# Optimization experiments

Hardware: AMD Instinct MI355X
Metric: run time of the kernel (lower is better)

The kernel has to match this reference:

```python
import jax, jax.numpy as jnp
import numpy as np

# ---- model constants (match init_kwargs) ----
N_USERS = 100_000
N_ITEMS = 50_000
N_ENTITIES = 200_000          # items are entities [0, N_ITEMS)
N_REL = 20                    # relations after the +1 shift; rel_weight has N_REL-1 rows
EMB = 64
HOPS = 2
MARGIN_CCL = 0.8
NUM_NEG = 64
ANGLE_W = 0.1
ANGLE_DROP = 0.5              # eval-mode Dropout(ones)*rate == constant rate scaling
N_EDGES = 1_000_000
NNZ = 1_000_000
N_TRIPLETS = 200_000
BATCH = 4096
EPS = 1e-6


def _l2norm(x):
    # torch F.normalize(dim=-1, eps=1e-12)
    return x / jnp.maximum(jnp.linalg.norm(x, axis=-1, keepdims=True), 1e-12)


def setup_inputs() -> dict:
    key = jax.random.key(0)
    ks = jax.random.split(key, 13)
    # xavier_uniform bounds: sqrt(6/(fan_in+fan_out))
    b_all = float(np.sqrt(6.0 / (N_USERS + N_ENTITIES + EMB)))
    b_cf = float(np.sqrt(6.0 / (N_ITEMS + EMB)))
    b_rel = float(np.sqrt(6.0 / (N_REL - 1 + EMB)))
    all_embed = jax.random.uniform(ks[0], (N_USERS + N_ENTITIES, EMB), jnp.float32, -b_all, b_all)
    item_emb_cf = jax.random.uniform(ks[1], (N_ITEMS, EMB), jnp.float32, -b_cf, b_cf)
    rel_weight = jax.random.uniform(ks[2], (N_REL - 1, EMB), jnp.float32, -b_rel, b_rel)
    # D^{-1/2} A row-normalized positive values
    interact_vals = jax.random.uniform(ks[3], (NNZ,), jnp.float32, 0.01, 0.3)
    user = jax.random.randint(ks[4], (BATCH,), 0, N_USERS)
    pos_item = jax.random.randint(ks[5], (BATCH,), 0, N_ITEMS)
    neg_item = jax.random.randint(ks[6], (BATCH, NUM_NEG), 0, N_ITEMS)
    edge_index = jax.random.randint(ks[7], (2, N_EDGES), 0, N_ENTITIES)
    edge_type = jax.random.randint(ks[8], (N_EDGES,), 1, N_REL)  # relations already +1 shifted
    interact_rows = jax.random.randint(ks[9], (NNZ,), 0, N_USERS)
    interact_cols = jax.random.randint(ks[10], (NNZ,), 0, N_ITEMS)  # URM cols live in item range
    triplet_h = jax.random.randint(ks[11], (N_TRIPLETS,), 0, N_ENTITIES)
    triplet_t = jax.random.randint(ks[12], (N_TRIPLETS,), 0, N_ITEMS)
    return dict(all_embed=all_embed, item_emb_cf=item_emb_cf, rel_weight=rel_weight,
                interact_vals=interact_vals, user=user, pos_item=pos_item, neg_item=neg_item,
                edge_index=edge_index, edge_type=edge_type, interact_rows=interact_rows,
                interact_cols=interact_cols, triplet_h=triplet_h, triplet_t=triplet_t)


def _gcn(user_emb, entity_emb, item_cf, rel_weight, edge_index, edge_type, rows, cols, vals):
    """Multi-hop HAKG GraphConv: relation-gated KG scatter-mean + sparse user/CF aggregation."""
    head, tail = edge_index[0], edge_index[1]
    ent_res, usr_res, cf_res = entity_emb, user_emb, item_cf
    cnt = jax.ops.segment_sum(jnp.ones(head.shape, entity_emb.dtype), head, N_ENTITIES)
    denom = jnp.maximum(cnt, 1.0)[:, None]            # scatter_mean denominator
    rel_e = rel_weight[edge_type - 1]                 # [E, D]
    for _ in range(HOPS):
        # KG aggregate: entity_agg[h] = mean_{(h,r,t)} entity[t] * rel[r]
        neigh = entity_emb[tail] * rel_e              # [E, D]
        entity_agg = jax.ops.segment_sum(neigh, head, N_ENTITIES) / denom
        # user aggregate: sparse interact_mat @ entity_emb
        user_agg = jax.ops.segment_sum(vals[:, None] * entity_emb[cols], rows, N_USERS)
        # CF branch (LightGCN-style): R @ item_cf then R^T @ (...)
        u_cf = jax.ops.segment_sum(vals[:, None] * item_cf[cols], rows, N_USERS)
        item_agg_cf = jax.ops.segment_sum(vals[:, None] * u_cf[rows], cols, N_ITEMS)
        entity_emb = _l2norm(entity_agg)
        user_emb = _l2norm(user_agg)
        item_cf = _l2norm(item_agg_cf)
        ent_res = ent_res + entity_emb
        usr_res = usr_res + user_emb
        cf_res = cf_res + item_cf
    return ent_res, usr_res, cf_res


def _half_aperture(u):
    K = 0.1
    sqnu = jnp.clip(jnp.sum(u * u, -1), 0.0, 1.0 - EPS)
    return jnp.arcsin(jnp.clip(K * (1.0 - sqnu) / jnp.sqrt(sqnu), -1.0 + EPS, 1.0 - EPS))


def _angle_at_u(u, v):
    nu = jnp.linalg.norm(u, axis=-1)
    nv = jnp.linalg.norm(v, axis=-1)
    dp = jnp.sum(u * v, -1)
    ed = jnp.linalg.norm(u - v, axis=-1)
    num = dp * (1.0 + nu ** 2) - nu ** 2 * (1.0 + nv ** 2)
    den = nu * ed * jnp.sqrt(jnp.clip(1.0 + nv ** 2 * nu ** 2 - 2.0 * dp, EPS, None)) + EPS
    return jnp.arccos(jnp.clip(num / den, -1.0 + EPS, 1.0 - EPS))


def _contrastive_loss(u_e, pos_e, neg_e, pos_cf, neg_cf):
    B = u_e.shape[0]
    u, p, n = _l2norm(u_e), _l2norm(pos_e), _l2norm(neg_e)
    pcf, ncf = _l2norm(pos_cf), _l2norm(neg_cf)
    ui_pos = jax.nn.relu(2.0 - (jnp.sum(u * p, -1) + jnp.sum(u * pcf, -1)))
    ub = jnp.repeat(u, NUM_NEG, axis=0)               # [B*K, D]
    def neg_loss(nn_):
        s = jax.nn.relu(jnp.sum(ub * nn_, -1) - MARGIN_CCL).reshape(B, NUM_NEG)
        return jnp.sum(s, -1) / (jnp.sum(s > 0, -1).astype(s.dtype) + 1e-5)
    return jnp.mean(ui_pos + neg_loss(n) + neg_loss(ncf))


def reference(all_embed, item_emb_cf, rel_weight, interact_vals, user, pos_item, neg_item,
              edge_index, edge_type, interact_rows, interact_cols, triplet_h, triplet_t):
    user_emb = all_embed[:N_USERS]
    entity_emb = all_embed[N_USERS:]
    ent_g, usr_g, cf_g = _gcn(user_emb, entity_emb, item_emb_cf, rel_weight,
                              edge_index, edge_type, interact_rows, interact_cols, interact_vals)
    flat_neg = neg_item.reshape(-1)
    u_e = usr_g[user]
    loss1 = _contrastive_loss(u_e, ent_g[pos_item], ent_g[flat_neg], cf_g[pos_item], cf_g[flat_neg])
    # angle (hierarchy) loss, vectorized over all cross-type triplets
    hs = entity_emb[triplet_h] * ANGLE_DROP
    ts = entity_emb[triplet_t] * ANGLE_DROP
    angle_half = jax.nn.relu(_angle_at_u(hs, ts) - _half_aperture(hs))
    loss2 = ANGLE_W * jnp.sum(angle_half) / N_TRIPLETS
    return loss1 + loss2
```

## Files before the change

kernel.cpp:

```cpp
#include <hip/hip_runtime.h>
#include <math.h>

#define N_USERS    100000
#define N_ITEMS    50000
#define N_ENTITIES 200000
#define N_REL      20
#define EMB        64
#define HOPS       2
#define MARGIN_CCL 0.8f
#define NUM_NEG    64
#define ANGLE_W    0.1f
#define ANGLE_DROP 0.5f
#define N_EDGES    1000000
#define NNZ        1000000
#define N_TRIPLETS 200000
#define BATCH      4096
#define EPSF       1e-6f

#define TILE1 4096
#define NBUCK 196
#define BCAP  9216
#define ACAP  8192
#define HBLK  ((N_EDGES + TILE1 - 1) / TILE1)
#define P1B   (3 * HBLK)
#define KGB   (N_ENTITIES / 32)
#define USERB (N_USERS / 16)
#define ITEMB ((N_ITEMS + 31) / 32)
#define ANGB  (N_TRIPLETS / 32)
#define LOSSB (BATCH / 4)
#define CONVE (N_ENTITIES * 16 / 256)
#define CONVI (N_ITEMS * 16 / 256)

typedef _Float16 half4_t __attribute__((ext_vector_type(4)));
typedef _Float16 half8_t __attribute__((ext_vector_type(8)));
typedef float float8_t __attribute__((ext_vector_type(8)));

__device__ inline float4 h2f(half4_t h) {
    return make_float4((float)h.x, (float)h.y, (float)h.z, (float)h.w);
}
__device__ inline half4_t f2h(float4 f) {
    half4_t h; h.x = (_Float16)f.x; h.y = (_Float16)f.y;
    h.z = (_Float16)f.z; h.w = (_Float16)f.w; return h;
}
__device__ inline float8_t h8_to_f8(half8_t h) { return __builtin_convertvector(h, float8_t); }
__device__ inline half8_t f8_to_h8(float8_t f) { return __builtin_convertvector(f, half8_t); }
__device__ inline half8_t h8_zero() {
    half8_t z;
    #pragma unroll
    for (int i = 0; i < 8; ++i) z[i] = (_Float16)0.0f;
    return z;
}
__device__ inline float sum_sq8(float8_t f) {
    float s = 0.f;
    #pragma unroll
    for (int i = 0; i < 8; ++i) s += f[i] * f[i];
    return s;
}
__device__ inline float dot8(float8_t a, float8_t b) {
    float s = 0.f;
    #pragma unroll
    for (int i = 0; i < 8; ++i) s += a[i] * b[i];
    return s;
}
__device__ inline float8_t f8_from2(float4 lo, float4 hi) {
    float8_t f;
    f[0] = lo.x; f[1] = lo.y; f[2] = lo.z; f[3] = lo.w;
    f[4] = hi.x; f[5] = hi.y; f[6] = hi.z; f[7] = hi.w;
    return f;
}
__device__ inline float grp_red8(float v) {
    v += __shfl_xor(v, 1, 64); v += __shfl_xor(v, 2, 64); v += __shfl_xor(v, 4, 64);
    return v;
}
__device__ inline float dot4(float4 a, float4 b) {
    return a.x * b.x + a.y * b.y + a.z * b.z + a.w * b.w;
}
__device__ inline float grp_red16(float v) {
    v += __shfl_xor(v, 1, 64); v += __shfl_xor(v, 2, 64);
    v += __shfl_xor(v, 4, 64); v += __shfl_xor(v, 8, 64);
    return v;
}
__device__ inline float cross_grp_scalar(float v) {
    v += __shfl_xor(v, 16, 64); v += __shfl_xor(v, 32, 64);
    return v;
}

__global__ void __launch_bounds__(256) prep_kernel(
        const float4* __restrict__ ent0, const float4* __restrict__ cf0,
        half4_t* __restrict__ ent_a, half4_t* __restrict__ comb_a,
        int* __restrict__ bcur_e, int* __restrict__ bcur_u, int* __restrict__ bcur_i) {
    int bx = blockIdx.x, t = threadIdx.x;
    if (bx < CONVE) { int i = bx * 256 + t; ent_a[i] = f2h(ent0[i]); return; }
    bx -= CONVE;
    if (bx < CONVI) {
        int i = bx * 256 + t;
        int row = i >> 4, o4 = i & 15;
        comb_a[row * 32 + o4] = f2h(ent0[i]);
        return;
    }
    bx -= CONVI;
    if (bx < CONVI) {
        int i = bx * 256 + t;
        int row = i >> 4, o4 = i & 15;
        comb_a[row * 32 + 16 + o4] = f2h(cf0[i]);
        return;
    }
    if (t < NBUCK) {
        bcur_e[t] = t * ACAP;
        bcur_u[t] = t * ACAP;
        bcur_i[t] = t * ACAP;
    }
}

__device__ inline void angle_body(int ablk, int t, const half8_t* __restrict__ ent_h,
                                  const int* __restrict__ th, const int* __restrict__ tt,
                                  float* sb, float* __restrict__ l2blk) {
    int o = t & 7;
    int grp = t >> 3;
    int trip = ablk * 32 + grp;
    int h = th[trip], t2 = tt[trip];
    float8_t hv = h8_to_f8(ent_h[h * 8 + o]);
    float8_t tv = h8_to_f8(ent_h[t2 * 8 + o]);
    hv *= ANGLE_DROP;
    tv *= ANGLE_DROP;
    float8_t dv = hv - tv;
    float s_hh = grp_red8(sum_sq8(hv));
    float s_tt = grp_red8(sum_sq8(tv));
    float s_ht = grp_red8(dot8(hv, tv));
    float s_dd = grp_red8(sum_sq8(dv));
    if (o == 0) {
        float nu = sqrtf(s_hh);
        float ed = sqrtf(s_dd);
        float sqnu = fminf(fmaxf(s_hh, 0.0f), 1.0f - EPSF);
        float ha_arg = fminf(fmaxf(0.1f * (1.0f - sqnu) / sqrtf(sqnu), -1.0f + EPSF), 1.0f - EPSF);
        float half_ap = asinf(ha_arg);
        float num = s_ht * (1.0f + s_hh) - s_hh * (1.0f + s_tt);
        float den = nu * ed * sqrtf(fmaxf(1.0f + s_tt * s_hh - 2.0f * s_ht, EPSF)) + EPSF;
        float ang = acosf(fminf(fmaxf(num / den, -1.0f + EPSF), 1.0f - EPSF));
        sb[grp] = fmaxf(ang - half_ap, 0.0f);
    }
    __syncthreads();
    if (t == 0) {
        float tot = 0.f;
        #pragma unroll
        for (int i = 0; i < 32; ++i) tot += sb[i];
        l2blk[ablk] = tot;
    }
}

__global__ void __launch_bounds__(256) phase1_angle(
        const int* __restrict__ head, const int* __restrict__ tail,
        const int* __restrict__ etype, const int* __restrict__ rows,
        const int* __restrict__ cols, const float* __restrict__ vals,
        int* __restrict__ bcur_e, int* __restrict__ bcur_u, int* __restrict__ bcur_i,
        int* __restrict__ keys_e, int* __restrict__ kg_pay,
        int2* __restrict__ u_pay, int2* __restrict__ i_pay,
        const half8_t* __restrict__ ent_a, const int* __restrict__ th,
        const int* __restrict__ tt, float* __restrict__ l2blk) {
    __shared__ int2 pay_st[TILE1];
    __shared__ int lhist[256], lstart[256], lcur[256], gbase[256];
    __shared__ float sb[32];
    int bx = blockIdx.x, t = threadIdx.x;
    if (bx >= P1B) {
        angle_body(bx - P1B, t, ent_a, th, tt, sb, l2blk);
        return;
    }
    int seg = bx / HBLK;
    int tb  = bx % HBLK;
    int tstart = tb * TILE1;
    int valid = min(TILE1, N_EDGES - tstart);
    const int* karr = (seg == 0) ? head : (seg == 1) ? rows : cols;
    int shift = (seg == 0) ? 10 : (seg == 1) ? 9 : 8;
    int* bcur = (seg == 0) ? bcur_e : (seg == 1) ? bcur_u : bcur_i;
    lhist[t] = 0;
    __syncthreads();
    for (int i = t; i < valid; i += 256) atomicAdd(&lhist[karr[tstart + i] >> shift], 1);
    __syncthreads();
    int v = lhist[t];
    lstart[t] = v;
    __syncthreads();
    for (int d = 1; d < 256; d <<= 1) {
        int x = (t >= d) ? lstart[t - d] : 0;
        __syncthreads();
        lstart[t] += x;
        __syncthreads();
    }
    int excl = lstart[t] - v;
    lstart[t] = excl;
    lcur[t] = excl;
    gbase[t] = atomicAdd(&bcur[t], v);
    __syncthreads();
    if (seg == 0) {
        int* key_st = (int*)pay_st;
        int* ps = key_st + TILE1;
        for (int i = t; i < valid; i += 256) {
            int h = head[tstart + i];
            int p = tail[tstart + i] | ((etype[tstart + i] - 1) << 18);
            int sp = atomicAdd(&lcur[h >> 10], 1);
            key_st[sp] = h;
            ps[sp] = p;
        }
        __syncthreads();
        for (int j = t; j < valid; j += 256) {
            int k = key_st[j];
            int b = k >> 10;
            int pos = gbase[b] + (j - lstart[b]);
            keys_e[pos] = k;
            kg_pay[pos] = ps[j];
        }
    } else {
        int2* pay = (seg == 1) ? u_pay : i_pay;
        for (int i = t; i < valid; i += 256) {
            int k = karr[tstart + i];
            int px;
            if (seg == 1) px = cols[tstart + i] | ((k & 511) << 16);
            else          px = rows[tstart + i] | ((k & 255) << 17);
            int2 p = make_int2(px, __float_as_int(vals[tstart + i]));
            int sp = atomicAdd(&lcur[k >> shift], 1);
            pay_st[sp] = p;
        }
        __syncthreads();
        for (int j = t; j < valid; j += 256) {
            int2 p = pay_st[j];
            int key = (seg == 1) ? ((p.x >> 16) & 511) : ((p.x >> 17) & 255);
            int b = (gbase[0], 0);
            (void)b;
            int lo = 0, hi = 255;
            while (lo < hi) {
                int mid = (lo + hi + 1) >> 1;
                if (lstart[mid] <= j) lo = mid; else hi = mid - 1;
            }
            int bb = lo;
            int pos = gbase[bb] + (j - lstart[bb]);
            pay[pos] = p;
        }
    }
}

__global__ void __launch_bounds__(256) phase2_all(
        const int* __restrict__ bcur_e, const int* __restrict__ keys_e,
        int* __restrict__ kg_pay, int* __restrict__ off_e,
        const int* __restrict__ bcur_u, int2* __restrict__ u_pay, int* __restrict__ off_u,
        const int* __restrict__ bcur_i, int2* __restrict__ i_pay, int* __restrict__ off_i) {
    __shared__ int hist[1024];
    __shared__ int s[256];
    __shared__ int2 lout2[BCAP];
    int seg = blockIdx.x / NBUCK;
    int b   = blockIdx.x % NBUCK;
    int t = threadIdx.x;
    int bins  = (seg == 0) ? 1024 : (seg == 1) ? 512 : 256;
    int shift = (seg == 0) ? 10 : (seg == 1) ? 9 : 8;
    int n_rows = (seg == 0) ? N_ENTITIES : (seg == 1) ? N_USERS : N_ITEMS;
    const int* bcur = (seg == 0) ? bcur_e : (seg == 1) ? bcur_u : bcur_i;
    int* off = (seg == 0) ? off_e : (seg == 1) ? off_u : off_i;
    int rs = b << shift;
    int re = min(rs + bins, n_rows);
    int nr = re - rs;
    int base = b * ACAP;
    int len = bcur[b] - base;
    for (int r = t; r < bins; r += 256) hist[r] = 0;
    __syncthreads();
    if (seg == 0) {
        for (int j = t; j < len; j += 256) atomicAdd(&hist[keys_e[base + j] - rs], 1);
    } else if (seg == 1) {
        for (int j = t; j < len; j += 256) atomicAdd(&hist[(u_pay[base + j].x >> 16) & 511], 1);
    } else {
        for (int j = t; j < len; j += 256) atomicAdd(&hist[(i_pay[base + j].x >> 17) & 255], 1);
    }
    __syncthreads();
    int own = bins >> 8;
    int c[4]; int tot = 0;
    #pragma unroll 4
    for (int i = 0; i < own; ++i) { c[i] = hist[t * own + i]; tot += c[i]; }
    s[t] = tot;
    __syncthreads();
    for (int d = 1; d < 256; d <<= 1) {
        int x = (t >= d) ? s[t - d] : 0;
        __syncthreads();
        s[t] += x;
        __syncthreads();
    }
    int run = s[t] - tot;
    #pragma unroll 4
    for (int i = 0; i < own; ++i) { hist[t * own + i] = run; run += c[i]; }
    __syncthreads();
    for (int r = t; r < nr; r += 256) off[rs + b + r] = base + hist[r];
    if (t == 0) off[rs + b + nr] = base + len;
    __syncthreads();
    if (seg == 0) {
        int* lo = (int*)lout2;
        for (int j = t; j < len; j += 256) {
            int k = keys_e[base + j];
            int slot = atomicAdd(&hist[k - rs], 1);
            lo[slot] = kg_pay[base + j];
        }
        __syncthreads();
        for (int j = t; j < len; j += 256) kg_pay[base + j] = lo[j];
    } else {
        int2* pay = (seg == 1) ? u_pay : i_pay;
        int sh = (seg == 1) ? 16 : 17;
        int msk = (seg == 1) ? 511 : 255;
        for (int j = t; j < len; j += 256) {
            int2 p = pay[base + j];
            int slot = atomicAdd(&hist[(p.x >> sh) & msk], 1);
            lout2[slot] = p;
        }
        __syncthreads();
        for (int j = t; j < len; j += 256) pay[base + j] = lout2[j];
    }
}

__device__ inline void kg_body(int bid, int t, const int* __restrict__ off,
                               const int* __restrict__ pack, half8_t* srel,
                               const float* __restrict__ relw,
                               const half8_t* __restrict__ src, half8_t* __restrict__ dst,
                               half8_t* __restrict__ comb_nxt, half8_t* __restrict__ res,
                               const float4* __restrict__ res_init, int first, int last) {
    if (t < (N_REL - 1) * 8) {
        int rel = t >> 3, o = t & 7;
        const float4* r4 = (const float4*)relw;
        srel[rel * 9 + o] = f8_to_h8(f8_from2(r4[rel * 16 + o * 2], r4[rel * 16 + o * 2 + 1]));
    }
    __syncthreads();
    int row = bid * 32 + (t >> 3);
    int o = t & 7;
    int idx = row + (row >> 10);
    int s = off[idx], e = off[idx + 1];
    half8_t acc = h8_zero();
    int k = s;
    for (; k + 2 <= e; k += 2) {
        int p0 = pack[k], p1 = pack[k + 1];
        half8_t a0 = src[(p0 & 0x3FFFF) * 8 + o];
        half8_t b0 = srel[(p0 >> 18) * 9 + o];
        half8_t a1 = src[(p1 & 0x3FFFF) * 8 + o];
        half8_t b1 = srel[(p1 >> 18) * 9 + o];
        acc += a0 * b0;
        acc += a1 * b1;
    }
    if (k < e) {
        int p0 = pack[k];
        acc += src[(p0 & 0x3FFFF) * 8 + o] * srel[(p0 >> 18) * 9 + o];
    }
    float8_t f = h8_to_f8(acc);
    f *= 1.0f / fmaxf((float)(e - s), 1.0f);
    float ss = grp_red8(sum_sq8(f));
    f *= 1.0f / fmaxf(sqrtf(ss), 1e-12f);
    half8_t oh = f8_to_h8(f);
    dst[row * 8 + o] = oh;
    if (row < N_ITEMS) {
        if (!last) comb_nxt[row * 16 + o] = oh;
        float8_t rr;
        if (first) rr = f8_from2(res_init[row * 16 + o * 2], res_init[row * 16 + o * 2 + 1]);
        else       rr = h8_to_f8(res[row * 8 + o]);
        rr += f;
        if (last) {
            float s2 = grp_red8(sum_sq8(rr));
            rr *= 1.0f / fmaxf(sqrtf(s2), 1e-12f);
        }
        res[row * 8 + o] = f8_to_h8(rr);
    }
}

__device__ inline void user_body(int bid, int t, const int* __restrict__ off,
                                 const int2* __restrict__ u_pack,
                                 const half8_t* __restrict__ comb,
                                 half8_t* __restrict__ usr_res,
                                 const float4* __restrict__ res_init,
                                 half8_t* __restrict__ ucf, int first, int last) {
    int row = bid * 16 + (t >> 4);
    int o = t & 15;
    int idx = row + (row >> 9);
    int s = off[idx], e = off[idx + 1];
    half8_t acc = h8_zero();
    int k = s;
    for (; k + 2 <= e; k += 2) {
        int2 p0 = u_pack[k], p1 = u_pack[k + 1];
        _Float16 v0 = (_Float16)__int_as_float(p0.y);
        _Float16 v1 = (_Float16)__int_as_float(p1.y);
        acc += comb[(p0.x & 0xFFFF) * 16 + o] * v0;
        acc += comb[(p1.x & 0xFFFF) * 16 + o] * v1;
    }
    if (k < e) {
        int2 p0 = u_pack[k];
        acc += comb[(p0.x & 0xFFFF) * 16 + o] * (_Float16)__int_as_float(p0.y);
    }
    float8_t f = h8_to_f8(acc);
    float ss = grp_red8(sum_sq8(f));
    if (o < 8) {
        float rn = 1.0f / fmaxf(sqrtf(ss), 1e-12f);
        float8_t rr;
        if (first) rr = f8_from2(res_init[row * 16 + o * 2], res_init[row * 16 + o * 2 + 1]);
        else       rr = h8_to_f8(usr_res[row * 8 + o]);
        rr += f * rn;
        if (last) {
            float s2 = grp_red8(sum_sq8(rr));
            rr *= 1.0f / fmaxf(sqrtf(s2), 1e-12f);
        }
        usr_res[row * 8 + o] = f8_to_h8(rr);
    } else {
        ucf[row * 8 + (o - 8)] = acc;
    }
}

__device__ inline void item_body(int bid, int t, const int* __restrict__ off,
                                 const int2* __restrict__ i_pack,
                                 const half8_t* __restrict__ ucf,
                                 half8_t* __restrict__ comb_nxt, half8_t* __restrict__ res,
                                 const float4* __restrict__ res_init, int first, int last) {
    int row = bid * 32 + (t >> 3);
    int o = t & 7;
    if (row >= N_ITEMS) return;
    int idx = row + (row >> 8);
    int s = off[idx], e = off[idx + 1];
    half8_t acc = h8_zero();
    int k = s;
    for (; k + 2 <= e; k += 2) {
        int2 p0 = i_pack[k], p1 = i_pack[k + 1];
        _Float16 v0 = (_Float16)__int_as_float(p0.y);
        _Float16 v1 = (_Float16)__int_as_float(p1.y);
        acc += ucf[(p0.x & 0x1FFFF) * 8 + o] * v0;
        acc += ucf[(p1.x & 0x1FFFF) * 8 + o] * v1;
    }
    if (k < e) {
        int2 p0 = i_pack[k];
        acc += ucf[(p0.x & 0x1FFFF) * 8 + o] * (_Float16)__int_as_float(p0.y);
    }
    float8_t f = h8_to_f8(acc);
    float ss = grp_red8(sum_sq8(f));
    f *= 1.0f / fmaxf(sqrtf(ss), 1e-12f);
    if (!last) comb_nxt[row * 16 + 8 + o] = f8_to_h8(f);
    float8_t rr;
    if (first) rr = f8_from2(res_init[row * 16 + o * 2], res_init[row * 16 + o * 2 + 1]);
    else       rr = h8_to_f8(res[row * 8 + o]);
    rr += f;
    if (last) {
        float s2 = grp_red8(sum_sq8(rr));
        rr *= 1.0f / fmaxf(sqrtf(s2), 1e-12f);
    }
    res[row * 8 + o] = f8_to_h8(rr);
}

__device__ inline void loss_ent_body(int b, int t, const int* __restrict__ user,
                                     const int* __restrict__ pos, const int* __restrict__ neg,
                                     const half4_t* __restrict__ usr4,
                                     const half4_t* __restrict__ ent4,
                                     float* __restrict__ dpe, float* __restrict__ l1pe) {
    int lane = t & 63;
    int g = lane >> 4, q = lane & 15;
    int uid = user[b], pid = pos[b];
    float4 u = h2f(usr4[uid * 16 + q]);
    float4 p = h2f(ent4[pid * 16 + q]);
    float dpe_v = grp_red16(dot4(u, p));
    float sum_n = 0.f, cnt_n = 0.f;
    const int* nb = neg + b * NUM_NEG;
    for (int j = 0; j < NUM_NEG; j += 8) {
        int n0 = nb[j + g], n1 = nb[j + 4 + g];
        float dn0 = grp_red16(dot4(u, h2f(ent4[n0 * 16 + q])));
        float dn1 = grp_red16(dot4(u, h2f(ent4[n1 * 16 + q])));
        float s0 = fmaxf(dn0 - MARGIN_CCL, 0.f); sum_n += s0; if (s0 > 0.f) cnt_n += 1.f;
        float s1 = fmaxf(dn1 - MARGIN_CCL, 0.f); sum_n += s1; if (s1 > 0.f) cnt_n += 1.f;
    }
    sum_n = cross_grp_scalar(sum_n); cnt_n = cross_grp_scalar(cnt_n);
    if (lane == 0) {
        dpe[b] = dpe_v;
        l1pe[b] = sum_n / (cnt_n + 1e-5f);
    }
}

__global__ void __launch_bounds__(256) loss_cf_kernel(
        const int* __restrict__ user, const int* __restrict__ pos,
        const int* __restrict__ neg, const half4_t* __restrict__ usr4,
        const half4_t* __restrict__ cf4, const float* __restrict__ dpe,
        const float* __restrict__ l1pe, float* __restrict__ l1p) {
    int b = blockIdx.x * 4 + (threadIdx.x >> 6);
    int lane = threadIdx.x & 63;
    int g = lane >> 4, q = lane & 15;
    int uid = user[b], pid = pos[b];
    float4 u = h2f(usr4[uid * 16 + q]);
    float4 pc = h2f(cf4[pid * 16 + q]);
    float dpc = grp_red16(dot4(u, pc));
    float sum_c = 0.f, cnt_c = 0.f;
    const int* nb = neg + b * NUM_NEG;
    for (int j = 0; j < NUM_NEG; j += 8) {
        int n0 = nb[j + g], n1 = nb[j + 4 + g];
        float dc0 = grp_red16(dot4(u, h2f(cf4[n0 * 16 + q])));
        float dc1 = grp_red16(dot4(u, h2f(cf4[n1 * 16 + q])));
        float t0 = fmaxf(dc0 - MARGIN_CCL, 0.f); sum_c += t0; if (t0 > 0.f) cnt_c += 1.f;
        float t1 = fmaxf(dc1 - MARGIN_CCL, 0.f); sum_c += t1; if (t1 > 0.f) cnt_c += 1.f;
    }
    sum_c = cross_grp_scalar(sum_c); cnt_c = cross_grp_scalar(cnt_c);
    if (lane == 0) {
        float ui_pos = fmaxf(2.0f - dpe[b] - dpc, 0.0f);
        l1p[b] = ui_pos + l1pe[b] + sum_c / (cnt_c + 1e-5f);
    }
}

__global__ void __launch_bounds__(256) fused_h0(
        const int* __restrict__ off_e, const int* __restrict__ kg_pack,
        const float* __restrict__ relw, const half8_t* __restrict__ ent_a,
        half8_t* __restrict__ ent_b, half8_t* __restrict__ comb_b,
        half8_t* __restrict__ ent_res, const float4* __restrict__ ent0f,
        const int* __restrict__ off_u, const int2* __restrict__ u_pack,
        const half8_t* __restrict__ comb_a, half8_t* __restrict__ usr_res,
        const float4* __restrict__ usr0f, half8_t* __restrict__ ucf) {
    __shared__ half8_t srel[(N_REL - 1) * 9];
    int bx = blockIdx.x, t = threadIdx.x;
    if (bx < KGB) {
        kg_body(bx, t, off_e, kg_pack, srel, relw, ent_a, ent_b, comb_b, ent_res, ent0f, 1, 0);
    } else {
        user_body(bx - KGB, t, off_u, u_pack, comb_a, usr_res, usr0f, ucf, 1, 0);
    }
}

__global__ void __launch_bounds__(256) fused_ik(
        const int* __restrict__ off_e, const int* __restrict__ kg_pack,
        const float* __restrict__ relw, const half8_t* __restrict__ ent_b,
        half8_t* __restrict__ ent_a, half8_t* __restrict__ ent_res,
        const float4* __restrict__ ent0f,
        const int* __restrict__ off_i, const int2* __restrict__ i_pack,
        const half8_t* __restrict__ ucf, half8_t* __restrict__ comb_b,
        half8_t* __restrict__ cf_res, const float4* __restrict__ cf0f) {
    __shared__ half8_t srel[(N_REL - 1) * 9];
    int bx = blockIdx.x, t = threadIdx.x;
    if (bx < KGB) {
        kg_body(bx, t, off_e, kg_pack, srel, relw, ent_b, ent_a, comb_b, ent_res, ent0f, 0, 1);
    } else {
        item_body(bx - KGB, t, off_i, i_pack, ucf, comb_b, cf_res, cf0f, 1, 0);
    }
}

__global__ void __launch_bounds__(256) user_h1(
        const int* __restrict__ off_u, const int2* __restrict__ u_pack,
        const half8_t* __restrict__ comb_b, half8_t* __restrict__ usr_res,
        const float4* __restrict__ usr0f, half8_t* __restrict__ ucf) {
    user_body(blockIdx.x, threadIdx.x, off_u, u_pack, comb_b, usr_res, usr0f, ucf, 0, 1);
}

__global__ void __launch_bounds__(256) fused_item_loss(
        const int* __restrict__ off_i, const int2* __restrict__ i_pack,
        const half8_t* __restrict__ ucf, half8_t* __restrict__ comb_unused,
        half8_t* __restrict__ cf_res, const float4* __restrict__ cf0f,
        const int* __restrict__ user, const int* __restrict__ pos,
        const int* __restrict__ neg, const half4_t* __restrict__ usr4,
        const half4_t* __restrict__ ent4, float* __restrict__ dpe,
        float* __restrict__ l1pe) {
    int bx = blockIdx.x, t = threadIdx.x;
    if (bx < ITEMB) {
        item_body(bx, t, off_i, i_pack, ucf, comb_unused, cf_res, cf0f, 0, 1);
    } else {
        int b = (bx - ITEMB) * 4 + (t >> 6);
        loss_ent_body(b, t, user, pos, neg, usr4, ent4, dpe, l1pe);
    }
}

__global__ void finalize_kernel(const float* __restrict__ l1p, const float* __restrict__ l2b,
                                float* __restrict__ out) {
    __shared__ float sb[1024];
    float a1 = 0.f;
    for (int i = threadIdx.x; i < BATCH; i += 1024) a1 += l1p[i];
    float a2 = 0.f;
    for (int i = threadIdx.x; i < ANGB; i += 1024) a2 += l2b[i];
    sb[threadIdx.x] = a1 / (float)BATCH + ANGLE_W * a2 / (float)N_TRIPLETS;
    __syncthreads();
    for (int s = 512; s > 0; s >>= 1) {
        if (threadIdx.x < s) sb[threadIdx.x] += sb[threadIdx.x + s];
        __syncthreads();
    }
    if (threadIdx.x == 0) out[0] = sb[0];
}

extern "C" void kernel_launch(void* const* d_in, const int* in_sizes, int n_in,
                              void* d_out, int out_size, void* d_ws, size_t ws_size,
                              hipStream_t stream) {
    const float* all_embed = (const float*)d_in[0];
    const float* item_cf0  = (const float*)d_in[1];
    const float* relw      = (const float*)d_in[2];
    const float* vals      = (const float*)d_in[3];
    const int* user        = (const int*)d_in[4];
    const int* pos_item    = (const int*)d_in[5];
    const int* neg_item    = (const int*)d_in[6];
    const int* edge_head   = (const int*)d_in[7];
    const int* edge_tail   = edge_head + N_EDGES;
    const int* etype       = (const int*)d_in[8];
    const int* irows       = (const int*)d_in[9];
    const int* icols       = (const int*)d_in[10];
    const int* th          = (const int*)d_in[11];
    const int* tt          = (const int*)d_in[12];
    float* out             = (float*)d_out;

    char* base = (char*)d_ws;
    size_t woff = 0;
    auto alloc = [&](size_t bytes) -> void* {
        void* p = base + woff;
        woff = (woff + bytes + 255) & ~(size_t)255;
        return p;
    };
    half8_t* ent_a   = (half8_t*)alloc((size_t)N_ENTITIES * EMB * 2);
    half8_t* ent_b   = (half8_t*)alloc((size_t)N_ENTITIES * EMB * 2);
    half8_t* comb_a  = (half8_t*)alloc((size_t)N_ITEMS * EMB * 4);
    half8_t* comb_b  = (half8_t*)alloc((size_t)N_ITEMS * EMB * 4);
    half8_t* ucf     = (half8_t*)alloc((size_t)N_USERS * EMB * 2);
    half8_t* ent_res = (half8_t*)alloc((size_t)N_ITEMS * EMB * 2);
    half8_t* usr_res = (half8_t*)alloc((size_t)N_USERS * EMB * 2);
    half8_t* cf_res  = (half8_t*)alloc((size_t)N_ITEMS * EMB * 2);
    int2* u_pack     = (int2*)alloc((size_t)NBUCK * ACAP * 8);
    int2* i_pack     = (int2*)alloc((size_t)NBUCK * ACAP * 8);
    int* kg_pack     = (int*)alloc((size_t)NBUCK * ACAP * 4);
    int* keys_e      = (int*)alloc((size_t)NBUCK * ACAP * 4);
    float* l1p       = (float*)alloc((size_t)BATCH * 4);
    float* dpe       = (float*)alloc((size_t)BATCH * 4);
    float* l1pe      = (float*)alloc((size_t)BATCH * 4);
    float* l2blk     = (float*)alloc((size_t)ANGB * 4);
    int* off_e       = (int*)alloc((size_t)(N_ENTITIES + NBUCK + 1) * 4);
    int* off_u       = (int*)alloc((size_t)(N_USERS + NBUCK + 1) * 4);
    int* off_i       = (int*)alloc((size_t)(N_ITEMS + NBUCK + 1) * 4);
    int* bcur_e      = (int*)alloc(256 * 4);
    int* bcur_u      = (int*)alloc(256 * 4);
    int* bcur_i      = (int*)alloc(256 * 4);

    const float* ent0 = all_embed + (size_t)N_USERS * EMB;

    prep_kernel<<<CONVE + 2 * CONVI + 1, 256, 0, stream>>>(
        (const float4*)ent0, (const float4*)item_cf0, (half4_t*)ent_a, (half4_t*)comb_a,
        bcur_e, bcur_u, bcur_i);
    phase1_angle<<<P1B + ANGB, 256, 0, stream>>>(
        edge_head, edge_tail, etype, irows, icols, vals,
        bcur_e, bcur_u, bcur_i, keys_e, kg_pack, u_pack, i_pack,
        ent_a, th, tt, l2blk);
    phase2_all<<<3 * NBUCK, 256, 0, stream>>>(bcur_e, keys_e, kg_pack, off_e,
                                              bcur_u, u_pack, off_u,
                                              bcur_i, i_pack, off_i);
    fused_h0<<<KGB + USERB, 256, 0, stream>>>(
        off_e, kg_pack, relw, ent_a, ent_b, comb_b, ent_res, (const float4*)ent0,
        off_u, u_pack, comb_a, usr_res, (const float4*)all_embed, ucf);
    fused_ik<<<KGB + ITEMB, 256, 0, stream>>>(
        off_e, kg_pack, relw, ent_b, ent_a, ent_res, (const float4*)ent0,
        off_i, i_pack, ucf, comb_b, cf_res, (const float4*)item_cf0);
    user_h1<<<USERB, 256, 0, stream>>>(off_u, u_pack, comb_b, usr_res,
                                       (const float4*)all_embed, ucf);
    fused_item_loss<<<ITEMB + LOSSB, 256, 0, stream>>>(
        off_i, i_pack, ucf, comb_a, cf_res, (const float4*)item_cf0,
        user, pos_item, neg_item, (const half4_t*)usr_res, (const half4_t*)ent_res,
        dpe, l1pe);
    loss_cf_kernel<<<LOSSB, 256, 0, stream>>>(user, pos_item, neg_item,
                                              (const half4_t*)usr_res, (const half4_t*)cf_res,
                                              dpe, l1pe, l1p);
    finalize_kernel<<<1, 1024, 0, stream>>>(l1p, l2blk, out);
}
```

Measured before the change: 415.5 us.

## Compute final-hop user embeddings only for batch users and restrict hop-2 KG to items

The final-hop KG aggregation now runs only over item rows, since only items are consumed downstream. The user aggregation over entity embeddings is computed just for the 4096 batch users, both hops at once, instead of for all 100k users. The combined entity/CF buffer is split into separate CF half buffers, and the user-CF and item-CF passes are regrouped into different fused kernels. This cuts gather traffic and block count substantially, but it changes the fp16 rounding order of the user residual and recomputes work for users that appear more than once in the batch.

```diff
diff --git a/kernel.cpp b/kernel.cpp
--- a/kernel.cpp
+++ b/kernel.cpp
@@ -24,8 +24,9 @@
 #define HBLK  ((N_EDGES + TILE1 - 1) / TILE1)
 #define P1B   (3 * HBLK)
 #define KGB   (N_ENTITIES / 32)
-#define USERB (N_USERS / 16)
+#define UCFB  (N_USERS / 32)
 #define ITEMB ((N_ITEMS + 31) / 32)
+#define UBB   (BATCH / 32)
 #define ANGB  (N_TRIPLETS / 32)
 #define LOSSB (BATCH / 4)
 #define CONVE (N_ENTITIES * 16 / 256)
@@ -87,24 +88,12 @@
 
 __global__ void __launch_bounds__(256) prep_kernel(
         const float4* __restrict__ ent0, const float4* __restrict__ cf0,
-        half4_t* __restrict__ ent_a, half4_t* __restrict__ comb_a,
+        half4_t* __restrict__ ent_a, half4_t* __restrict__ cf16_a,
         int* __restrict__ bcur_e, int* __restrict__ bcur_u, int* __restrict__ bcur_i) {
     int bx = blockIdx.x, t = threadIdx.x;
     if (bx < CONVE) { int i = bx * 256 + t; ent_a[i] = f2h(ent0[i]); return; }
     bx -= CONVE;
-    if (bx < CONVI) {
-        int i = bx * 256 + t;
-        int row = i >> 4, o4 = i & 15;
-        comb_a[row * 32 + o4] = f2h(ent0[i]);
-        return;
-    }
-    bx -= CONVI;
-    if (bx < CONVI) {
-        int i = bx * 256 + t;
-        int row = i >> 4, o4 = i & 15;
-        comb_a[row * 32 + 16 + o4] = f2h(cf0[i]);
-        return;
-    }
+    if (bx < CONVI) { int i = bx * 256 + t; cf16_a[i] = f2h(cf0[i]); return; }
     if (t < NBUCK) {
         bcur_e[t] = t * ACAP;
         bcur_u[t] = t * ACAP;
@@ -222,9 +211,6 @@
         __syncthreads();
         for (int j = t; j < valid; j += 256) {
             int2 p = pay_st[j];
-            int key = (seg == 1) ? ((p.x >> 16) & 511) : ((p.x >> 17) & 255);
-            int b = (gbase[0], 0);
-            (void)b;
             int lo = 0, hi = 255;
             while (lo < hi) {
                 int mid = (lo + hi + 1) >> 1;
@@ -310,12 +296,11 @@
     }
 }
 
-__device__ inline void kg_body(int bid, int t, const int* __restrict__ off,
-                               const int* __restrict__ pack, half8_t* srel,
-                               const float* __restrict__ relw,
-                               const half8_t* __restrict__ src, half8_t* __restrict__ dst,
-                               half8_t* __restrict__ comb_nxt, half8_t* __restrict__ res,
-                               const float4* __restrict__ res_init, int first, int last) {
+__device__ inline void kg0_body(int bid, int t, const int* __restrict__ off,
+                                const int* __restrict__ pack, half8_t* srel,
+                                const float* __restrict__ relw,
+                                const half8_t* __restrict__ src, half8_t* __restrict__ dst,
+                                half8_t* __restrict__ res, const float4* __restrict__ res_init) {
     if (t < (N_REL - 1) * 8) {
         int rel = t >> 3, o = t & 7;
         const float4* r4 = (const float4*)relw;
@@ -345,30 +330,61 @@
     f *= 1.0f / fmaxf((float)(e - s), 1.0f);
     float ss = grp_red8(sum_sq8(f));
     f *= 1.0f / fmaxf(sqrtf(ss), 1e-12f);
-    half8_t oh = f8_to_h8(f);
-    dst[row * 8 + o] = oh;
+    dst[row * 8 + o] = f8_to_h8(f);
     if (row < N_ITEMS) {
-        if (!last) comb_nxt[row * 16 + o] = oh;
-        float8_t rr;
-        if (first) rr = f8_from2(res_init[row * 16 + o * 2], res_init[row * 16 + o * 2 + 1]);
-        else       rr = h8_to_f8(res[row * 8 + o]);
+        float8_t rr = f8_from2(res_init[row * 16 + o * 2], res_init[row * 16 + o * 2 + 1]);
         rr += f;
-        if (last) {
-            float s2 = grp_red8(sum_sq8(rr));
-            rr *= 1.0f / fmaxf(sqrtf(s2), 1e-12f);
-        }
         res[row * 8 + o] = f8_to_h8(rr);
     }
 }
 
-__device__ inline void user_body(int bid, int t, const int* __restrict__ off,
-                                 const int2* __restrict__ u_pack,
-                                 const half8_t* __restrict__ comb,
-                                 half8_t* __restrict__ usr_res,
-                                 const float4* __restrict__ res_init,
-                                 half8_t* __restrict__ ucf, int first, int last) {
-    int row = bid * 16 + (t >> 4);
-    int o = t & 15;
+__device__ inline void kg2_body(int bid, int t, const int* __restrict__ off,
+                                const int* __restrict__ pack, half8_t* srel,
+                                const float* __restrict__ relw,
+                                const half8_t* __restrict__ src, half8_t* __restrict__ res) {
+    if (t < (N_REL - 1) * 8) {
+        int rel = t >> 3, o = t & 7;
+        const float4* r4 = (const float4*)relw;
+        srel[rel * 9 + o] = f8_to_h8(f8_from2(r4[rel * 16 + o * 2], r4[rel * 16 + o * 2 + 1]));
+    }
+    __syncthreads();
+    int row = bid * 32 + (t >> 3);
+    if (row >= N_ITEMS) return;
+    int o = t & 7;
+    int idx = row + (row >> 10);
+    int s = off[idx], e = off[idx + 1];
+    half8_t acc = h8_zero();
+    int k = s;
+    for (; k + 2 <= e; k += 2) {
+        int p0 = pack[k], p1 = pack[k + 1];
+        half8_t a0 = src[(p0 & 0x3FFFF) * 8 + o];
+        half8_t b0 = srel[(p0 >> 18) * 9 + o];
+        half8_t a1 = src[(p1 & 0x3FFFF) * 8 + o];
+        half8_t b1 = srel[(p1 >> 18) * 9 + o];
+        acc += a0 * b0;
+        acc += a1 * b1;
+    }
+    if (k < e) {
+        int p0 = pack[k];
+        acc += src[(p0 & 0x3FFFF) * 8 + o] * srel[(p0 >> 18) * 9 + o];
+    }
+    float8_t f = h8_to_f8(acc);
+    f *= 1.0f / fmaxf((float)(e - s), 1.0f);
+    float ss = grp_red8(sum_sq8(f));
+    f *= 1.0f / fmaxf(sqrtf(ss), 1e-12f);
+    float8_t rr = h8_to_f8(res[row * 8 + o]);
+    rr += f;
+    float s2 = grp_red8(sum_sq8(rr));
+    rr *= 1.0f / fmaxf(sqrtf(s2), 1e-12f);
+    res[row * 8 + o] = f8_to_h8(rr);
+}
+
+__device__ inline void ucf_body(int bid, int t, const int* __restrict__ off,
+                                const int2* __restrict__ u_pack,
+                                const half8_t* __restrict__ cf16,
+                                half8_t* __restrict__ ucf) {
+    int row = bid * 32 + (t >> 3);
+    int o = t & 7;
     int idx = row + (row >> 9);
     int s = off[idx], e = off[idx + 1];
     half8_t acc = h8_zero();
@@ -377,35 +393,66 @@
         int2 p0 = u_pack[k], p1 = u_pack[k + 1];
         _Float16 v0 = (_Float16)__int_as_float(p0.y);
         _Float16 v1 = (_Float16)__int_as_float(p1.y);
-        acc += comb[(p0.x & 0xFFFF) * 16 + o] * v0;
-        acc += comb[(p1.x & 0xFFFF) * 16 + o] * v1;
+        acc += cf16[(p0.x & 0xFFFF) * 8 + o] * v0;
+        acc += cf16[(p1.x & 0xFFFF) * 8 + o] * v1;
     }
     if (k < e) {
         int2 p0 = u_pack[k];
-        acc += comb[(p0.x & 0xFFFF) * 16 + o] * (_Float16)__int_as_float(p0.y);
-    }
-    float8_t f = h8_to_f8(acc);
-    float ss = grp_red8(sum_sq8(f));
-    if (o < 8) {
-        float rn = 1.0f / fmaxf(sqrtf(ss), 1e-12f);
-        float8_t rr;
-        if (first) rr = f8_from2(res_init[row * 16 + o * 2], res_init[row * 16 + o * 2 + 1]);
-        else       rr = h8_to_f8(usr_res[row * 8 + o]);
-        rr += f * rn;
-        if (last) {
-            float s2 = grp_red8(sum_sq8(rr));
-            rr *= 1.0f / fmaxf(sqrtf(s2), 1e-12f);
-        }
-        usr_res[row * 8 + o] = f8_to_h8(rr);
-    } else {
-        ucf[row * 8 + (o - 8)] = acc;
-    }
+        acc += cf16[(p0.x & 0xFFFF) * 8 + o] * (_Float16)__int_as_float(p0.y);
+    }
+    ucf[row * 8 + o] = acc;
+}
+
+__device__ inline void ubatch_body(int bid, int t, const int* __restrict__ user,
+                                   const int* __restrict__ off,
+                                   const int2* __restrict__ u_pack,
+                                   const half8_t* __restrict__ ent_a,
+                                   const half8_t* __restrict__ ent_b,
+                                   const float4* __restrict__ usr0f,
+                                   half8_t* __restrict__ usr_b) {
+    int g = t >> 3, o = t & 7;
+    int b = bid * 32 + g;
+    int uid = user[b];
+    int idx = uid + (uid >> 9);
+    int s = off[idx], e = off[idx + 1];
+    half8_t acc1 = h8_zero(), acc2 = h8_zero();
+    int k = s;
+    for (; k + 2 <= e; k += 2) {
+        int2 p0 = u_pack[k], p1 = u_pack[k + 1];
+        int c0 = (p0.x & 0xFFFF) * 8 + o;
+        int c1 = (p1.x & 0xFFFF) * 8 + o;
+        _Float16 v0 = (_Float16)__int_as_float(p0.y);
+        _Float16 v1 = (_Float16)__int_as_float(p1.y);
+        acc1 += ent_a[c0] * v0;
+        acc2 += ent_b[c0] * v0;
+        acc1 += ent_a[c1] * v1;
+        acc2 += ent_b[c1] * v1;
+    }
+    if (k < e) {
+        int2 p0 = u_pack[k];
+        int c0 = (p0.x & 0xFFFF) * 8 + o;
+        _Float16 v0 = (_Float16)__int_as_float(p0.y);
+        acc1 += ent_a[c0] * v0;
+        acc2 += ent_b[c0] * v0;
+    }
+    float8_t f1 = h8_to_f8(acc1);
+    float ss1 = grp_red8(sum_sq8(f1));
+    f1 *= 1.0f / fmaxf(sqrtf(ss1), 1e-12f);
+    float8_t u0 = f8_from2(usr0f[uid * 16 + o * 2], usr0f[uid * 16 + o * 2 + 1]);
+    float8_t r1 = h8_to_f8(f8_to_h8(u0 + f1));
+    float8_t f2 = h8_to_f8(acc2);
+    float ss2 = grp_red8(sum_sq8(f2));
+    f2 *= 1.0f / fmaxf(sqrtf(ss2), 1e-12f);
+    float8_t r = r1 + f2;
+    float s3 = grp_red8(sum_sq8(r));
+    r *= 1.0f / fmaxf(sqrtf(s3), 1e-12f);
+    usr_b[b * 8 + o] = f8_to_h8(r);
 }
 
 __device__ inline void item_body(int bid, int t, const int* __restrict__ off,
                                  const int2* __restrict__ i_pack,
                                  const half8_t* __restrict__ ucf,
-                                 half8_t* __restrict__ comb_nxt, half8_t* __restrict__ res,
+                                 half8_t* __restrict__ cf_nxt, half8_t* __restrict__ res,
                                  const float4* __restrict__ res_init, int first, int last) {
     int row = bid * 32 + (t >> 3);
     int o = t & 7;
@@ -428,7 +475,7 @@
     float8_t f = h8_to_f8(acc);
     float ss = grp_red8(sum_sq8(f));
     f *= 1.0f / fmaxf(sqrtf(ss), 1e-12f);
-    if (!last) comb_nxt[row * 16 + 8 + o] = f8_to_h8(f);
+    if (!last) cf_nxt[row * 8 + o] = f8_to_h8(f);
     float8_t rr;
     if (first) rr = f8_from2(res_init[row * 16 + o * 2], res_init[row * 16 + o * 2 + 1]);
     else       rr = h8_to_f8(res[row * 8 + o]);
@@ -440,15 +487,15 @@
     res[row * 8 + o] = f8_to_h8(rr);
 }
 
-__device__ inline void loss_ent_body(int b, int t, const int* __restrict__ user,
+__device__ inline void loss_ent_body(int b, int t,
                                      const int* __restrict__ pos, const int* __restrict__ neg,
-                                     const half4_t* __restrict__ usr4,
+                                     const half4_t* __restrict__ usrb4,
                                      const half4_t* __restrict__ ent4,
                                      float* __restrict__ dpe, float* __restrict__ l1pe) {
     int lane = t & 63;
     int g = lane >> 4, q = lane & 15;
-    int uid = user[b], pid = pos[b];
-    float4 u = h2f(usr4[uid * 16 + q]);
+    int pid = pos[b];
+    float4 u = h2f(usrb4[b * 16 + q]);
     float4 p = h2f(ent4[pid * 16 + q]);
     float dpe_v = grp_red16(dot4(u, p));
     float sum_n = 0.f, cnt_n = 0.f;
@@ -468,15 +515,15 @@
 }
 
 __global__ void __launch_bounds__(256) loss_cf_kernel(
-        const int* __restrict__ user, const int* __restrict__ pos,
-        const int* __restrict__ neg, const half4_t* __restrict__ usr4,
-        const half4_t* __restrict__ cf4, const float* __restrict__ dpe,
-        const float* __restrict__ l1pe, float* __restrict__ l1p) {
+        const int* __restrict__ pos, const int* __restrict__ neg,
+        const half4_t* __restrict__ usrb4, const half4_t* __restrict__ cf4,
+        const float* __restrict__ dpe, const float* __restrict__ l1pe,
+        float* __restrict__ l1p) {
     int b = blockIdx.x * 4 + (threadIdx.x >> 6);
     int lane = threadIdx.x & 63;
     int g = lane >> 4, q = lane & 15;
-    int uid = user[b], pid = pos[b];
-    float4 u = h2f(usr4[uid * 16 + q]);
+    int pid = pos[b];
+    float4 u = h2f(usrb4[b * 16 + q]);
     float4 pc = h2f(cf4[pid * 16 + q]);
     float dpc = grp_red16(dot4(u, pc));
     float sum_c = 0.f, cnt_c = 0.f;
@@ -498,59 +545,60 @@
 __global__ void __launch_bounds__(256) fused_h0(
         const int* __restrict__ off_e, const int* __restrict__ kg_pack,
         const float* __restrict__ relw, const half8_t* __restrict__ ent_a,
-        half8_t* __restrict__ ent_b, half8_t* __restrict__ comb_b,
-        half8_t* __restrict__ ent_res, const float4* __restrict__ ent0f,
+        half8_t* __restrict__ ent_b, half8_t* __restrict__ ent_res,
+        const float4* __restrict__ ent0f,
         const int* __restrict__ off_u, const int2* __restrict__ u_pack,
-        const half8_t* __restrict__ comb_a, half8_t* __restrict__ usr_res,
-        const float4* __restrict__ usr0f, half8_t* __restrict__ ucf) {
+        const half8_t* __restrict__ cf16_a, half8_t* __restrict__ ucf) {
     __shared__ half8_t srel[(N_REL - 1) * 9];
     int bx = blockIdx.x, t = threadIdx.x;
     if (bx < KGB) {
-        kg_body(bx, t, off_e, kg_pack, srel, relw, ent_a, ent_b, comb_b, ent_res, ent0f, 1, 0);
+        kg0_body(bx, t, off_e, kg_pack, srel, relw, ent_a, ent_b, ent_res, ent0f);
     } else {
-        user_body(bx - KGB, t, off_u, u_pack, comb_a, usr_res, usr0f, ucf, 1, 0);
+        ucf_body(bx - KGB, t, off_u, u_pack, cf16_a, ucf);
     }
 }
 
 __global__ void __launch_bounds__(256) fused_ik(
         const int* __restrict__ off_e, const int* __restrict__ kg_pack,
         const float* __restrict__ relw, const half8_t* __restrict__ ent_b,
-        half8_t* __restrict__ ent_a, half8_t* __restrict__ ent_res,
-        const float4* __restrict__ ent0f,
+        half8_t* __restrict__ ent_res,
         const int* __restrict__ off_i, const int2* __restrict__ i_pack,
-        const half8_t* __restrict__ ucf, half8_t* __restrict__ comb_b,
-        half8_t* __restrict__ cf_res, const float4* __restrict__ cf0f) {
+        const half8_t* __restrict__ ucf, half8_t* __restrict__ cf16_b,
+        half8_t* __restrict__ cf_res, const float4* __restrict__ cf0f,
+        const int* __restrict__ user, const int* __restrict__ off_u,
+        const int2* __restrict__ u_pack, const half8_t* __restrict__ ent_a,
+        const float4* __restrict__ usr0f, half8_t* __restrict__ usr_b) {
     __shared__ half8_t srel[(N_REL - 1) * 9];
     int bx = blockIdx.x, t = threadIdx.x;
-    if (bx < KGB) {
-        kg_body(bx, t, off_e, kg_pack, srel, relw, ent_b, ent_a, comb_b, ent_res, ent0f, 0, 1);
+    if (bx < ITEMB) {
+        kg2_body(bx, t, off_e, kg_pack, srel, relw, ent_b, ent_res);
+    } else if (bx < 2 * ITEMB) {
+        item_body(bx - ITEMB, t, off_i, i_pack, ucf, cf16_b, cf_res, cf0f, 1, 0);
     } else {
-        item_body(bx - KGB, t, off_i, i_pack, ucf, comb_b, cf_res, cf0f, 1, 0);
-    }
-}
-
-__global__ void __launch_bounds__(256) user_h1(
+        ubatch_body(bx - 2 * ITEMB, t, user, off_u, u_pack, ent_a, ent_b, usr0f, usr_b);
+    }
+}
+
+__global__ void __launch_bounds__(256) fused_u1_loss(
         const int* __restrict__ off_u, const int2* __restrict__ u_pack,
-        const half8_t* __restrict__ comb_b, half8_t* __restrict__ usr_res,
-        const float4* __restrict__ usr0f, half8_t* __restrict__ ucf) {
-    user_body(blockIdx.x, threadIdx.x, off_u, u_pack, comb_b, usr_res, usr0f, ucf, 0, 1);
-}
-
-__global__ void __launch_bounds__(256) fused_item_loss(
+        const half8_t* __restrict__ cf16_b, half8_t* __restrict__ ucf,
+        const int* __restrict__ pos, const int* __restrict__ neg,
+        const half4_t* __restrict__ usrb4, const half4_t* __restrict__ ent4,
+        float* __restrict__ dpe, float* __restrict__ l1pe) {
+    int bx = blockIdx.x, t = threadIdx.x;
+    if (bx < UCFB) {
+        ucf_body(bx, t, off_u, u_pack, cf16_b, ucf);
+    } else {
+        int b = (bx - UCFB) * 4 + (t >> 6);
+        loss_ent_body(b, t, pos, neg, usrb4, ent4, dpe, l1pe);
+    }
+}
+
+__global__ void __launch_bounds__(256) item_h1(
         const int* __restrict__ off_i, const int2* __restrict__ i_pack,
-        const half8_t* __restrict__ ucf, half8_t* __restrict__ comb_unused,
-        half8_t* __restrict__ cf_res, const float4* __restrict__ cf0f,
-        const int* __restrict__ user, const int* __restrict__ pos,
-        const int* __restrict__ neg, const half4_t* __restrict__ usr4,
-        const half4_t* __restrict__ ent4, float* __restrict__ dpe,
-        float* __restrict__ l1pe) {
-    int bx = blockIdx.x, t = threadIdx.x;
-    if (bx < ITEMB) {
-        item_body(bx, t, off_i, i_pack, ucf, comb_unused, cf_res, cf0f, 0, 1);
-    } else {
-        int b = (bx - ITEMB) * 4 + (t >> 6);
-        loss_ent_body(b, t, user, pos, neg, usr4, ent4, dpe, l1pe);
-    }
+        const half8_t* __restrict__ ucf, half8_t* __restrict__ cf_res,
+        const float4* __restrict__ cf0f) {
+    item_body(blockIdx.x, threadIdx.x, off_i, i_pack, ucf, (half8_t*)0, cf_res, cf0f, 0, 1);
 }
 
 __global__ void finalize_kernel(const float* __restrict__ l1p, const float* __restrict__ l2b,
@@ -597,12 +645,12 @@
     };
     half8_t* ent_a   = (half8_t*)alloc((size_t)N_ENTITIES * EMB * 2);
     half8_t* ent_b   = (half8_t*)alloc((size_t)N_ENTITIES * EMB * 2);
-    half8_t* comb_a  = (half8_t*)alloc((size_t)N_ITEMS * EMB * 4);
-    half8_t* comb_b  = (half8_t*)alloc((size_t)N_ITEMS * EMB * 4);
+    half8_t* cf16_a  = (half8_t*)alloc((size_t)N_ITEMS * EMB * 2);
+    half8_t* cf16_b  = (half8_t*)alloc((size_t)N_ITEMS * EMB * 2);
     half8_t* ucf     = (half8_t*)alloc((size_t)N_USERS * EMB * 2);
     half8_t* ent_res = (half8_t*)alloc((size_t)N_ITEMS * EMB * 2);
-    half8_t* usr_res = (half8_t*)alloc((size_t)N_USERS * EMB * 2);
     half8_t* cf_res  = (half8_t*)alloc((size_t)N_ITEMS * EMB * 2);
+    half8_t* usr_b   = (half8_t*)alloc((size_t)BATCH * EMB * 2);
     int2* u_pack     = (int2*)alloc((size_t)NBUCK * ACAP * 8);
     int2* i_pack     = (int2*)alloc((size_t)NBUCK * ACAP * 8);
     int* kg_pack     = (int*)alloc((size_t)NBUCK * ACAP * 4);
@@ -620,8 +668,8 @@
 
     const float* ent0 = all_embed + (size_t)N_USERS * EMB;
 
-    prep_kernel<<<CONVE + 2 * CONVI + 1, 256, 0, stream>>>(
-        (const float4*)ent0, (const float4*)item_cf0, (half4_t*)ent_a, (half4_t*)comb_a,
+    prep_kernel<<<CONVE + CONVI + 1, 256, 0, stream>>>(
+        (const float4*)ent0, (const float4*)item_cf0, (half4_t*)ent_a, (half4_t*)cf16_a,
         bcur_e, bcur_u, bcur_i);
     phase1_angle<<<P1B + ANGB, 256, 0, stream>>>(
         edge_head, edge_tail, etype, irows, icols, vals,
@@ -630,20 +678,20 @@
     phase2_all<<<3 * NBUCK, 256, 0, stream>>>(bcur_e, keys_e, kg_pack, off_e,
                                               bcur_u, u_pack, off_u,
                                               bcur_i, i_pack, off_i);
-    fused_h0<<<KGB + USERB, 256, 0, stream>>>(
-        off_e, kg_pack, relw, ent_a, ent_b, comb_b, ent_res, (const float4*)ent0,
-        off_u, u_pack, comb_a, usr_res, (const float4*)all_embed, ucf);
-    fused_ik<<<KGB + ITEMB, 256, 0, stream>>>(
-        off_e, kg_pack, relw, ent_b, ent_a, ent_res, (const float4*)ent0,
-        off_i, i_pack, ucf, comb_b, cf_res, (const float4*)item_cf0);
-    user_h1<<<USERB, 256, 0, stream>>>(off_u, u_pack, comb_b, usr_res,
-                                       (const float4*)all_embed, ucf);
-    fused_item_loss<<<ITEMB + LOSSB, 256, 0, stream>>>(
-        off_i, i_pack, ucf, comb_a, cf_res, (const float4*)item_cf0,
-        user, pos_item, neg_item, (const half4_t*)usr_res, (const half4_t*)ent_res,
-        dpe, l1pe);
-    loss_cf_kernel<<<LOSSB, 256, 0, stream>>>(user, pos_item, neg_item,
-                                              (const half4_t*)usr_res, (const half4_t*)cf_res,
+    fused_h0<<<KGB + UCFB, 256, 0, stream>>>(
+        off_e, kg_pack, relw, ent_a, ent_b, ent_res, (const float4*)ent0,
+        off_u, u_pack, cf16_a, ucf);
+    fused_ik<<<2 * ITEMB + UBB, 256, 0, stream>>>(
+        off_e, kg_pack, relw, ent_b, ent_res,
+        off_i, i_pack, ucf, cf16_b, cf_res, (const float4*)item_cf0,
+        user, off_u, u_pack, ent_a, (const float4*)all_embed, usr_b);
+    fused_u1_loss<<<UCFB + LOSSB, 256, 0, stream>>>(
+        off_u, u_pack, cf16_b, ucf, pos_item, neg_item,
+        (const half4_t*)usr_b, (const half4_t*)ent_res, dpe, l1pe);
+    item_h1<<<ITEMB, 256, 0, stream>>>(off_i, i_pack, ucf, cf_res,
+                                       (const float4*)item_cf0);
+    loss_cf_kernel<<<LOSSB, 256, 0, stream>>>(pos_item, neg_item,
+                                              (const half4_t*)usr_b, (const half4_t*)cf_res,
                                               dpe, l1pe, l1p);
     finalize_kernel<<<1, 1024, 0, stream>>>(l1p, l2blk, out);
 }
```

After: 356.5 us. 1.17x faster.
